# Performance work log

Measured on AMD Instinct MI355X. Metric: run time of the kernel, lower is better.

## Reference

```python
import jax, jax.numpy as jnp
import numpy as np

N_NODES = 1_000_000
IN_DIM = 128
HID = 256
NCLS = 47
N0, N1, N2 = 1_171_456, 45_056, 4_096
F0, F1 = 25, 10


def setup_inputs() -> dict:
    key = jax.random.key(0)
    ks = jax.random.split(key, 8)
    s_in = 1.0 / np.sqrt(IN_DIM)
    s_h = 1.0 / np.sqrt(HID)
    return {
        "node_feat": jax.random.normal(ks[0], (N_NODES, IN_DIM), jnp.float32),
        "gid0": jax.random.randint(ks[1], (N0,), 0, N_NODES, jnp.int64 if jax.config.jax_enable_x64 else jnp.int32),
        "col0": jax.random.randint(ks[2], (N1 * F0,), 0, N0),
        "col1": jax.random.randint(ks[3], (N2 * F1,), 0, N1),
        "Wn0": jax.random.normal(ks[4], (IN_DIM, HID), jnp.float32) * s_in,
        "Wr0": jax.random.normal(ks[5], (IN_DIM, HID), jnp.float32) * s_in,
        "b0": jnp.zeros((HID,), jnp.float32),
        "Wn1": jax.random.normal(ks[6], (HID, NCLS), jnp.float32) * s_h,
        "Wr1": jax.random.normal(ks[7], (HID, NCLS), jnp.float32) * s_h,
        "b1": jnp.zeros((NCLS,), jnp.float32),
    }


def _sage_layer(x_src, col, n_dst, fanout, Wn, Wr, b):
    # mean aggregation over fixed-fanout sampled neighbors (CSR with uniform rows)
    neigh = x_src[col].reshape(n_dst, fanout, x_src.shape[-1]).mean(axis=1)
    return neigh @ Wn + x_src[:n_dst] @ Wr + b


def reference(node_feat, gid0, col0, col1, Wn0, Wr0, b0, Wn1, Wr1, b1):
    x = node_feat[gid0]                      # [N0, IN_DIM] embedding gather
    x = _sage_layer(x, col0, N1, F0, Wn0, Wr0, b0)   # [N1, HID]
    x = jax.nn.relu(x)                       # dropout = identity (eval mode)
    out = _sage_layer(x, col1, N2, F1, Wn1, Wr1, b1) # [N2, NCLS]
    return out
```

## Files before the change

kernel.cpp:

```cpp
#include <hip/hip_runtime.h>
#include <hip/hip_bf16.h>
#include <stdint.h>

#define NNODES  1000000
#define INDIM   128
#define HIDDIM  256
#define NCLSN   47
#define N0SZ    1171456
#define N1SZ    45056
#define N2SZ    4096
#define F0SZ    25
#define F1SZ    10

typedef __attribute__((ext_vector_type(8))) short short8;
typedef __attribute__((ext_vector_type(4))) float f32x4;

__device__ inline unsigned short f2bfu(float x) {
    union { __hip_bfloat16 h; unsigned short u; } cv;
    cv.h = __float2bfloat16(x);
    return cv.u;
}

__device__ inline float bfu2f(unsigned short u) {
    union { float f; unsigned int u; } cv;
    cv.u = ((unsigned int)u) << 16;
    return cv.f;
}

__global__ __launch_bounds__(256) void prep_kernel(
    const float* __restrict__ Wn0, const float* __restrict__ Wr0,
    const float* __restrict__ Wn1, const float* __restrict__ Wr1,
    const int* __restrict__ gid0, const int* __restrict__ col0,
    __hip_bfloat16* __restrict__ W0T, __hip_bfloat16* __restrict__ W1T,
    int* __restrict__ fidx, int* __restrict__ sidx,
    int* __restrict__ mask, int* __restrict__ list, int* __restrict__ nlive) {
    const int tid = blockIdx.x * 256 + threadIdx.x;
    if (tid < 256 * 256) {
        int n = tid >> 8, k = tid & 255;
        float v = (k < INDIM) ? Wn0[(size_t)k * HIDDIM + n] : Wr0[(size_t)(k - INDIM) * HIDDIM + n];
        W0T[(size_t)n * 256 + k] = __float2bfloat16(v);
    }
    if (tid < 48 * 512) {
        int n = tid / 512, k = tid % 512;
        float v = 0.f;
        if (n < NCLSN) v = (k < HIDDIM) ? Wn1[(size_t)k * NCLSN + n] : Wr1[(size_t)(k - HIDDIM) * NCLSN + n];
        W1T[(size_t)n * 512 + k] = __float2bfloat16(v);
    }
    if (tid < N1SZ) {
        sidx[tid] = gid0[tid];
        mask[tid] = (tid < N2SZ) ? 1 : 0;
    }
    if (tid < N2SZ) list[tid] = tid;
    if (tid == 0) *nlive = N2SZ;
    if (tid < N1SZ * F0SZ) fidx[tid] = gid0[col0[tid]];
}

__global__ __launch_bounds__(256) void mark_kernel(
    const int* __restrict__ col1, int* __restrict__ mask,
    int* __restrict__ list, int* __restrict__ nlive) {
    const int t = blockIdx.x * 256 + threadIdx.x;
    if (t < N2SZ * F1SZ) {
        int c = col1[t];
        if (atomicExch(&mask[c], 1) == 0) {
            int k = atomicAdd(nlive, 1);
            list[k] = c;
        }
    }
}

__global__ __launch_bounds__(256) void fused_layer0_kernel(
    const float* __restrict__ node_feat, const int* __restrict__ fidx,
    const int* __restrict__ sidx, const int* __restrict__ list,
    const int* __restrict__ nlive, const __hip_bfloat16* __restrict__ W0T,
    const float* __restrict__ b0, __hip_bfloat16* __restrict__ H) {
    __shared__ int sg[16 * F0SZ];
    __shared__ int sself[16];
    __shared__ int slist[16];
    __shared__ alignas(16) short Atile[16 * 264];

    const int tid = threadIdx.x;
    const int rowbase = blockIdx.x * 16;
    const int nl = *nlive;
    if (rowbase >= nl) return;

    if (tid < 16) {
        int idx = rowbase + tid;
        int row = (idx < nl) ? list[idx] : -1;
        slist[tid] = row;
        sself[tid] = (row >= 0) ? sidx[row] : 0;
    }
    for (int t = tid; t < 16 * F0SZ; t += 256) {
        int idx = rowbase + t / F0SZ;
        sg[t] = (idx < nl) ? fidx[(size_t)list[idx] * F0SZ + t % F0SZ] : 0;
    }
    __syncthreads();

    {
        const int r = tid >> 4;
        const int l = tid & 15;
        const bool live = (slist[r] >= 0);
        float a0 = 0.f, a1 = 0.f, a2 = 0.f, a3 = 0.f, a4 = 0.f, a5 = 0.f, a6 = 0.f, a7 = 0.f;
        float4 s0 = make_float4(0.f, 0.f, 0.f, 0.f);
        float4 s1 = make_float4(0.f, 0.f, 0.f, 0.f);
        if (live) {
            #pragma unroll
            for (int f = 0; f < F0SZ; ++f) {
                const float* p = node_feat + (size_t)sg[r * F0SZ + f] * INDIM + l * 8;
                float4 v0 = ((const float4*)p)[0];
                float4 v1 = ((const float4*)p)[1];
                a0 += v0.x; a1 += v0.y; a2 += v0.z; a3 += v0.w;
                a4 += v1.x; a5 += v1.y; a6 += v1.z; a7 += v1.w;
            }
            const float* sp = node_feat + (size_t)sself[r] * INDIM + l * 8;
            s0 = ((const float4*)sp)[0];
            s1 = ((const float4*)sp)[1];
        }
        const float s = 1.0f / F0SZ;
        short8 m;
        m[0] = f2bfu(a0 * s); m[1] = f2bfu(a1 * s); m[2] = f2bfu(a2 * s); m[3] = f2bfu(a3 * s);
        m[4] = f2bfu(a4 * s); m[5] = f2bfu(a5 * s); m[6] = f2bfu(a6 * s); m[7] = f2bfu(a7 * s);
        *(short8*)&Atile[r * 264 + l * 8] = m;
        short8 se;
        se[0] = f2bfu(s0.x); se[1] = f2bfu(s0.y); se[2] = f2bfu(s0.z); se[3] = f2bfu(s0.w);
        se[4] = f2bfu(s1.x); se[5] = f2bfu(s1.y); se[6] = f2bfu(s1.z); se[7] = f2bfu(s1.w);
        *(short8*)&Atile[r * 264 + 128 + l * 8] = se;
    }
    __syncthreads();

    {
        const int wid = tid >> 6;
        const int lane = tid & 63;
        const int l15 = lane & 15;
        const int g = lane >> 4;
        const int nbase = wid * 64;
        const short* B = (const short*)W0T;
        f32x4 acc[4] = {};
        #pragma unroll
        for (int kk = 0; kk < 256; kk += 32) {
            const int ka = kk + g * 8;
            short8 a = *(const short8*)&Atile[l15 * 264 + ka];
            #pragma unroll
            for (int nt = 0; nt < 4; ++nt) {
                short8 b = *(const short8*)(B + (size_t)(nbase + nt * 16 + l15) * 256 + ka);
                acc[nt] = __builtin_amdgcn_mfma_f32_16x16x32_bf16(a, b, acc[nt], 0, 0, 0);
            }
        }
        #pragma unroll
        for (int nt = 0; nt < 4; ++nt) {
            const int col = nbase + nt * 16 + l15;
            const float bias = b0[col];
            #pragma unroll
            for (int r = 0; r < 4; ++r) {
                const int row = slist[g * 4 + r];
                if (row >= 0) {
                    float v = acc[nt][r] + bias;
                    v = v > 0.f ? v : 0.f;
                    H[(size_t)row * HIDDIM + col] = __float2bfloat16(v);
                }
            }
        }
    }
}

__global__ __launch_bounds__(512) void fused_layer1_kernel(
    const __hip_bfloat16* __restrict__ H, const int* __restrict__ col1,
    const __hip_bfloat16* __restrict__ W1T, const float* __restrict__ b1,
    float* __restrict__ out) {
    __shared__ int sc[16 * F1SZ];
    __shared__ alignas(16) short Xtile[16 * 520];
    __shared__ alignas(16) float red[8][16 * 48];

    const int tid = threadIdx.x;
    const int rowbase = blockIdx.x * 16;

    if (tid < 16 * F1SZ) {
        int i = rowbase + tid / F1SZ;
        int f = tid % F1SZ;
        sc[tid] = col1[(size_t)i * F1SZ + f];
    }
    __syncthreads();

    {
        const int r = tid >> 5;
        const int l = tid & 31;
        const unsigned short* Hs = (const unsigned short*)H;
        float a0 = 0.f, a1 = 0.f, a2 = 0.f, a3 = 0.f, a4 = 0.f, a5 = 0.f, a6 = 0.f, a7 = 0.f;
        #pragma unroll
        for (int f = 0; f < F1SZ; ++f) {
            const unsigned short* p = Hs + (size_t)sc[r * F1SZ + f] * HIDDIM + l * 8;
            ushort4 v0 = ((const ushort4*)p)[0];
            ushort4 v1 = ((const ushort4*)p)[1];
            a0 += bfu2f(v0.x); a1 += bfu2f(v0.y); a2 += bfu2f(v0.z); a3 += bfu2f(v0.w);
            a4 += bfu2f(v1.x); a5 += bfu2f(v1.y); a6 += bfu2f(v1.z); a7 += bfu2f(v1.w);
        }
        const float s = 1.0f / F1SZ;
        short8 m;
        m[0] = f2bfu(a0 * s); m[1] = f2bfu(a1 * s); m[2] = f2bfu(a2 * s); m[3] = f2bfu(a3 * s);
        m[4] = f2bfu(a4 * s); m[5] = f2bfu(a5 * s); m[6] = f2bfu(a6 * s); m[7] = f2bfu(a7 * s);
        *(short8*)&Xtile[r * 520 + l * 8] = m;
        short8 se = *(const short8*)((const short*)Hs + (size_t)(rowbase + r) * HIDDIM + l * 8);
        *(short8*)&Xtile[r * 520 + 256 + l * 8] = se;
    }
    __syncthreads();

    {
        const int wid = tid >> 6;
        const int lane = tid & 63;
        const int l15 = lane & 15;
        const int g = lane >> 4;
        const short* B = (const short*)W1T;
        f32x4 acc[3] = {};
        const int kbase = wid * 64;
        #pragma unroll
        for (int ks = 0; ks < 2; ++ks) {
            const int ka = kbase + ks * 32 + g * 8;
            short8 a = *(const short8*)&Xtile[l15 * 520 + ka];
            #pragma unroll
            for (int nt = 0; nt < 3; ++nt) {
                short8 b = *(const short8*)(B + (size_t)(nt * 16 + l15) * 512 + ka);
                acc[nt] = __builtin_amdgcn_mfma_f32_16x16x32_bf16(a, b, acc[nt], 0, 0, 0);
            }
        }
        #pragma unroll
        for (int nt = 0; nt < 3; ++nt)
            #pragma unroll
            for (int rr = 0; rr < 4; ++rr)
                red[wid][(g * 4 + rr) * 48 + nt * 16 + l15] = acc[nt][rr];
    }
    __syncthreads();

    for (int t = tid; t < 16 * 48; t += 512) {
        int rr = t / 48, c = t % 48;
        if (c < NCLSN) {
            float v = b1[c];
            #pragma unroll
            for (int w = 0; w < 8; ++w) v += red[w][t];
            out[(size_t)(rowbase + rr) * NCLSN + c] = v;
        }
    }
}

extern "C" void kernel_launch(void* const* d_in, const int* in_sizes, int n_in,
                              void* d_out, int out_size, void* d_ws, size_t ws_size,
                              hipStream_t stream) {
    const float* node_feat = (const float*)d_in[0];
    const int*   gid0      = (const int*)d_in[1];
    const int*   col0      = (const int*)d_in[2];
    const int*   col1      = (const int*)d_in[3];
    const float* Wn0       = (const float*)d_in[4];
    const float* Wr0       = (const float*)d_in[5];
    const float* b0        = (const float*)d_in[6];
    const float* Wn1       = (const float*)d_in[7];
    const float* Wr1       = (const float*)d_in[8];
    const float* b1        = (const float*)d_in[9];

    char* ws = (char*)d_ws;
    __hip_bfloat16* H    = (__hip_bfloat16*)(ws);
    __hip_bfloat16* W0T  = (__hip_bfloat16*)(ws + 23068672);
    __hip_bfloat16* W1T  = (__hip_bfloat16*)(ws + 23199744);
    int*            fidx = (int*)(ws + 23248896);
    int*            sidx = (int*)(ws + 27754496);
    int*            mask = (int*)(ws + 27934720);
    int*            list = (int*)(ws + 28114944);
    int*            nlive= (int*)(ws + 28295168);
    float* out = (float*)d_out;

    hipLaunchKernelGGL(prep_kernel, dim3(4400), dim3(256), 0, stream,
                       Wn0, Wr0, Wn1, Wr1, gid0, col0, W0T, W1T, fidx, sidx,
                       mask, list, nlive);
    hipLaunchKernelGGL(mark_kernel, dim3((N2SZ * F1SZ + 255) / 256), dim3(256), 0, stream,
                       col1, mask, list, nlive);
    hipLaunchKernelGGL(fused_layer0_kernel, dim3(N1SZ / 16), dim3(256), 0, stream,
                       node_feat, fidx, sidx, list, nlive, W0T, b0, H);
    hipLaunchKernelGGL(fused_layer1_kernel, dim3(N2SZ / 16), dim3(512), 0, stream,
                       H, col1, W1T, b1, out);
}
```

Before: 111.2 us.

## Compact neighbor index gather to live rows and widen layer0 blocks

Index precomputation (fidx/sidx) now runs after the live-row marking and covers only the live layer-1 nodes, written in compacted order. Before, it covered all N1*F0 entries. This cuts the dependent gid0[col0] gather work and lets layer0 read contiguous compacted indices. Layer0 blocks now handle 32 rows with 512 threads, so each block has two row halves sharing the weight tile. The reorder adds a dependency that serialises prep after mark.

```diff
diff --git a/kernel.cpp b/kernel.cpp
--- a/kernel.cpp
+++ b/kernel.cpp
@@ -27,32 +27,12 @@
     return cv.f;
 }
 
-__global__ __launch_bounds__(256) void prep_kernel(
-    const float* __restrict__ Wn0, const float* __restrict__ Wr0,
-    const float* __restrict__ Wn1, const float* __restrict__ Wr1,
-    const int* __restrict__ gid0, const int* __restrict__ col0,
-    __hip_bfloat16* __restrict__ W0T, __hip_bfloat16* __restrict__ W1T,
-    int* __restrict__ fidx, int* __restrict__ sidx,
+__global__ __launch_bounds__(256) void init_kernel(
     int* __restrict__ mask, int* __restrict__ list, int* __restrict__ nlive) {
     const int tid = blockIdx.x * 256 + threadIdx.x;
-    if (tid < 256 * 256) {
-        int n = tid >> 8, k = tid & 255;
-        float v = (k < INDIM) ? Wn0[(size_t)k * HIDDIM + n] : Wr0[(size_t)(k - INDIM) * HIDDIM + n];
-        W0T[(size_t)n * 256 + k] = __float2bfloat16(v);
-    }
-    if (tid < 48 * 512) {
-        int n = tid / 512, k = tid % 512;
-        float v = 0.f;
-        if (n < NCLSN) v = (k < HIDDIM) ? Wn1[(size_t)k * NCLSN + n] : Wr1[(size_t)(k - HIDDIM) * NCLSN + n];
-        W1T[(size_t)n * 512 + k] = __float2bfloat16(v);
-    }
-    if (tid < N1SZ) {
-        sidx[tid] = gid0[tid];
-        mask[tid] = (tid < N2SZ) ? 1 : 0;
-    }
+    if (tid < N1SZ) mask[tid] = (tid < N2SZ) ? 1 : 0;
     if (tid < N2SZ) list[tid] = tid;
     if (tid == 0) *nlive = N2SZ;
-    if (tid < N1SZ * F0SZ) fidx[tid] = gid0[col0[tid]];
 }
 
 __global__ __launch_bounds__(256) void mark_kernel(
@@ -68,30 +48,56 @@
     }
 }
 
-__global__ __launch_bounds__(256) void fused_layer0_kernel(
-    const float* __restrict__ node_feat, const int* __restrict__ fidx,
-    const int* __restrict__ sidx, const int* __restrict__ list,
+__global__ __launch_bounds__(256) void prep_kernel(
+    const float* __restrict__ Wn0, const float* __restrict__ Wr0,
+    const float* __restrict__ Wn1, const float* __restrict__ Wr1,
+    const int* __restrict__ gid0, const int* __restrict__ col0,
+    const int* __restrict__ list, const int* __restrict__ nlive,
+    __hip_bfloat16* __restrict__ W0T, __hip_bfloat16* __restrict__ W1T,
+    int* __restrict__ fidx_c, int* __restrict__ sidx_c) {
+    const int tid = blockIdx.x * 256 + threadIdx.x;
+    if (tid < 256 * 256) {
+        int n = tid >> 8, k = tid & 255;
+        float v = (k < INDIM) ? Wn0[(size_t)k * HIDDIM + n] : Wr0[(size_t)(k - INDIM) * HIDDIM + n];
+        W0T[(size_t)n * 256 + k] = __float2bfloat16(v);
+    }
+    if (tid < 48 * 512) {
+        int n = tid / 512, k = tid % 512;
+        float v = 0.f;
+        if (n < NCLSN) v = (k < HIDDIM) ? Wn1[(size_t)k * NCLSN + n] : Wr1[(size_t)(k - HIDDIM) * NCLSN + n];
+        W1T[(size_t)n * 512 + k] = __float2bfloat16(v);
+    }
+    const int nl = *nlive;
+    if (tid < nl) sidx_c[tid] = gid0[list[tid]];
+    if (tid < nl * F0SZ) {
+        int j = tid / F0SZ, f = tid % F0SZ;
+        fidx_c[tid] = gid0[col0[(size_t)list[j] * F0SZ + f]];
+    }
+}
+
+__global__ __launch_bounds__(512) void fused_layer0_kernel(
+    const float* __restrict__ node_feat, const int* __restrict__ fidx_c,
+    const int* __restrict__ sidx_c, const int* __restrict__ list,
     const int* __restrict__ nlive, const __hip_bfloat16* __restrict__ W0T,
     const float* __restrict__ b0, __hip_bfloat16* __restrict__ H) {
-    __shared__ int sg[16 * F0SZ];
-    __shared__ int sself[16];
-    __shared__ int slist[16];
-    __shared__ alignas(16) short Atile[16 * 264];
+    __shared__ int sg[32 * F0SZ];
+    __shared__ int sself[32];
+    __shared__ int slist[32];
+    __shared__ alignas(16) short Atile[32 * 264];
 
     const int tid = threadIdx.x;
-    const int rowbase = blockIdx.x * 16;
+    const int rowbase = blockIdx.x * 32;
     const int nl = *nlive;
     if (rowbase >= nl) return;
 
-    if (tid < 16) {
+    if (tid < 32) {
         int idx = rowbase + tid;
-        int row = (idx < nl) ? list[idx] : -1;
-        slist[tid] = row;
-        sself[tid] = (row >= 0) ? sidx[row] : 0;
-    }
-    for (int t = tid; t < 16 * F0SZ; t += 256) {
-        int idx = rowbase + t / F0SZ;
-        sg[t] = (idx < nl) ? fidx[(size_t)list[idx] * F0SZ + t % F0SZ] : 0;
+        slist[tid] = (idx < nl) ? list[idx] : -1;
+        sself[tid] = (idx < nl) ? sidx_c[idx] : 0;
+    }
+    for (int t = tid; t < 32 * F0SZ; t += 512) {
+        int e = rowbase * F0SZ + t;
+        sg[t] = (e < nl * F0SZ) ? fidx_c[e] : 0;
     }
     __syncthreads();
 
@@ -132,13 +138,14 @@
         const int lane = tid & 63;
         const int l15 = lane & 15;
         const int g = lane >> 4;
-        const int nbase = wid * 64;
+        const int rhalf = (wid >> 2) * 16;
+        const int nbase = (wid & 3) * 64;
         const short* B = (const short*)W0T;
         f32x4 acc[4] = {};
         #pragma unroll
         for (int kk = 0; kk < 256; kk += 32) {
             const int ka = kk + g * 8;
-            short8 a = *(const short8*)&Atile[l15 * 264 + ka];
+            short8 a = *(const short8*)&Atile[(rhalf + l15) * 264 + ka];
             #pragma unroll
             for (int nt = 0; nt < 4; ++nt) {
                 short8 b = *(const short8*)(B + (size_t)(nbase + nt * 16 + l15) * 256 + ka);
@@ -151,7 +158,7 @@
             const float bias = b0[col];
             #pragma unroll
             for (int r = 0; r < 4; ++r) {
-                const int row = slist[g * 4 + r];
+                const int row = slist[rhalf + g * 4 + r];
                 if (row >= 0) {
                     float v = acc[nt][r] + bias;
                     v = v > 0.f ? v : 0.f;
@@ -255,23 +262,25 @@
     const float* b1        = (const float*)d_in[9];
 
     char* ws = (char*)d_ws;
-    __hip_bfloat16* H    = (__hip_bfloat16*)(ws);
-    __hip_bfloat16* W0T  = (__hip_bfloat16*)(ws + 23068672);
-    __hip_bfloat16* W1T  = (__hip_bfloat16*)(ws + 23199744);
-    int*            fidx = (int*)(ws + 23248896);
-    int*            sidx = (int*)(ws + 27754496);
-    int*            mask = (int*)(ws + 27934720);
-    int*            list = (int*)(ws + 28114944);
-    int*            nlive= (int*)(ws + 28295168);
+    __hip_bfloat16* H     = (__hip_bfloat16*)(ws);
+    __hip_bfloat16* W0T   = (__hip_bfloat16*)(ws + 23068672);
+    __hip_bfloat16* W1T   = (__hip_bfloat16*)(ws + 23199744);
+    int*            fidx_c = (int*)(ws + 23248896);
+    int*            sidx_c = (int*)(ws + 27754496);
+    int*            mask   = (int*)(ws + 27934720);
+    int*            list   = (int*)(ws + 28114944);
+    int*            nlive  = (int*)(ws + 28295168);
     float* out = (float*)d_out;
 
-    hipLaunchKernelGGL(prep_kernel, dim3(4400), dim3(256), 0, stream,
-                       Wn0, Wr0, Wn1, Wr1, gid0, col0, W0T, W1T, fidx, sidx,
+    hipLaunchKernelGGL(init_kernel, dim3((N1SZ + 255) / 256), dim3(256), 0, stream,
                        mask, list, nlive);
     hipLaunchKernelGGL(mark_kernel, dim3((N2SZ * F1SZ + 255) / 256), dim3(256), 0, stream,
                        col1, mask, list, nlive);
-    hipLaunchKernelGGL(fused_layer0_kernel, dim3(N1SZ / 16), dim3(256), 0, stream,
-                       node_feat, fidx, sidx, list, nlive, W0T, b0, H);
+    hipLaunchKernelGGL(prep_kernel, dim3(4400), dim3(256), 0, stream,
+                       Wn0, Wr0, Wn1, Wr1, gid0, col0, list, nlive,
+                       W0T, W1T, fidx_c, sidx_c);
+    hipLaunchKernelGGL(fused_layer0_kernel, dim3((N1SZ + 31) / 32), dim3(512), 0, stream,
+                       node_feat, fidx_c, sidx_c, list, nlive, W0T, b0, H);
     hipLaunchKernelGGL(fused_layer1_kernel, dim3(N2SZ / 16), dim3(512), 0, stream,
                        H, col1, W1T, b1, out);
 }
```

Measured after the change: 128.2 us. 15.3% more time.
